# Performance work log

Measured on AMD Instinct MI355X. Metric: run time of the kernel, lower is better.

Reference implementation:

```python
import jax, jax.numpy as jnp
import numpy as np

NU, NI, ED, H = 30000, 10000, 64, 4
D = ED * H            # fusion_dim = 256
N = NU + NI           # total graph nodes
E = 100000            # edges
B = 8192              # scored (user, wine) pairs
NST, SD = 4, 64       # side tokens / side token dim
NEG = -1e30


def setup_inputs():
    key = jax.random.key(0)
    ks = iter(jax.random.split(key, 64))

    def w(*shape):
        return jax.random.normal(next(ks), shape, jnp.float32) * 0.05

    return {
        "user": jax.random.randint(next(ks), (B,), 0, NU),
        "wine": jax.random.randint(next(ks), (B,), 0, NI),
        "edge_index": jax.random.randint(next(ks), (2, E), 0, N),
        "keep_edge": jax.random.uniform(next(ks), (E,)) > 0.2,   # edge_dropout keep mask
        "node_mask": jax.random.uniform(next(ks), (N,)) < 0.2,   # mask-autoencoding mask
        "user_emb": w(NU, ED),
        "wine_emb": w(NI, ED),
        "up_w": w(ED, D), "up_b": w(D),
        "wp_w": w(ED, D), "wp_b": w(D),
        "sf_proj_w": w(SD, D), "sf_proj_b": w(D),
        "sf_q_w": w(D, D), "sf_q_b": w(D),
        "sf_k_w": w(D, D), "sf_k_b": w(D),
        "sf_v_w": w(D, D), "sf_v_b": w(D),
        "sf_o_w": w(D, D), "sf_o_b": w(D),
        "sf_fc_w": w(2 * D, D), "sf_fc_b": w(D),
        "g_w": w(D, D), "g_b": w(D),
        "t_q_w": w(D, H * D), "t_q_b": w(H * D),
        "t_k_w": w(D, H * D), "t_k_b": w(H * D),
        "t_v_w": w(D, H * D), "t_v_b": w(H * D),
        "t_skip_w": w(D, D), "t_skip_b": w(D),
        "fc_w": w(2 * D, 1), "fc_b": w(1),
        "ae_w": w(D, D), "ae_b": w(D),
        "ep_w": w(2 * D, 1), "ep_b": w(1),
        "wine_side_features": jax.random.normal(next(ks), (NI, NST, SD), jnp.float32),
    }


def _forward(user, wine, edge_index, keep_edge, node_mask,
             user_emb, wine_emb, up_w, up_b, wp_w, wp_b,
             sf_proj_w, sf_proj_b, sf_q_w, sf_q_b, sf_k_w, sf_k_b,
             sf_v_w, sf_v_b, sf_o_w, sf_o_b, sf_fc_w, sf_fc_b,
             g_w, g_b, t_q_w, t_q_b, t_k_w, t_k_b, t_v_w, t_v_b,
             t_skip_w, t_skip_b, fc_w, fc_b, ae_w, ae_b, ep_w, ep_b,
             wine_side_features):
    u_proj = user_emb @ up_w + up_b                       # [NU, D]
    w_proj = wine_emb @ wp_w + wp_b                       # [NI, D]

    # WineSideFusion: single-head attention of wine embedding over side tokens
    side = wine_side_features @ sf_proj_w + sf_proj_b     # [NI, T, D]
    q = w_proj @ sf_q_w + sf_q_b                          # [NI, D]
    k = side @ sf_k_w + sf_k_b                            # [NI, T, D]
    v = side @ sf_v_w + sf_v_b
    attn = jax.nn.softmax(jnp.einsum('nd,ntd->nt', q, k) / jnp.sqrt(jnp.float32(D)), axis=-1)
    ao = jnp.einsum('nt,ntd->nd', attn, v) @ sf_o_w + sf_o_b
    fused = jnp.concatenate([w_proj, ao], axis=1) @ sf_fc_w + sf_fc_b

    x = jnp.concatenate([u_proj, fused], axis=0)          # [N, D]
    src, dst = edge_index[0], edge_index[1]
    ew = keep_edge.astype(x.dtype)                        # edge dropout as 0/1 weights

    # GCNConv (add self loops, symmetric norm)
    deg = jax.ops.segment_sum(ew, dst, num_segments=N) + 1.0
    dinv = jax.lax.rsqrt(deg)
    norm = dinv[src] * dinv[dst] * ew                     # [E]
    xw = x @ g_w                                          # [N, D]
    agg = jax.ops.segment_sum(xw[src] * norm[:, None], dst, num_segments=N)
    x = agg + xw * (dinv * dinv)[:, None] + g_b

    # TransformerConv(heads=H, concat=False): mean over heads + skip
    qh = (x @ t_q_w + t_q_b).reshape(N, H, D)
    kh = (x @ t_k_w + t_k_b).reshape(N, H, D)
    vh = (x @ t_v_w + t_v_b).reshape(N, H, D)
    logits = jnp.einsum('ehd,ehd->eh', qh[dst], kh[src]) / jnp.sqrt(jnp.float32(D))
    logits = jnp.where(keep_edge[:, None], logits, NEG)
    m = jax.ops.segment_max(logits, dst, num_segments=N)  # [N, H]
    m = jnp.where(m < NEG / 2, 0.0, m)                    # guard empty segments
    e = jnp.exp(logits - m[dst]) * ew[:, None]            # [E, H]
    den = jax.ops.segment_sum(e, dst, num_segments=N)     # [N, H]
    num = jax.ops.segment_sum(e[:, :, None] * vh[src], dst, num_segments=N)  # [N, H, D]
    attn_out = num / jnp.maximum(den, 1e-16)[:, :, None]
    x = attn_out.mean(axis=1) + x @ t_skip_w + t_skip_b   # [N, D]

    # Masked autoencoding: masked rows are zeroed, then autoencoded -> recon = bias
    maskf = node_mask.astype(x.dtype)
    recon = ae_b                                          # 0 @ ae_w + ae_b
    diff = recon[None, :] - x                             # [N, D]
    recon_loss = jnp.sum(maskf[:, None] * diff * diff) / (jnp.sum(maskf) * D)

    u_out = x[user]                                       # [B, D]
    w_out = x[wine + NU]                                  # [B, D]
    pair = jnp.concatenate([u_out, w_out], axis=1)        # [B, 2D]

    edge_score = jax.nn.sigmoid(pair @ ep_w + ep_b)       # [B, 1]
    edge_pred_loss = jnp.mean((edge_score - 1.0) ** 2)

    score = jax.nn.sigmoid((pair @ fc_w + fc_b).squeeze(-1)) * 4.0 + 1.0  # [B]
    return score, recon_loss, edge_pred_loss


def reference(user, wine, edge_index, keep_edge, node_mask,
              user_emb, wine_emb, up_w, up_b, wp_w, wp_b,
              sf_proj_w, sf_proj_b, sf_q_w, sf_q_b, sf_k_w, sf_k_b,
              sf_v_w, sf_v_b, sf_o_w, sf_o_b, sf_fc_w, sf_fc_b,
              g_w, g_b, t_q_w, t_q_b, t_k_w, t_k_b, t_v_w, t_v_b,
              t_skip_w, t_skip_b, fc_w, fc_b, ae_w, ae_b, ep_w, ep_b,
              wine_side_features):
    return _forward(user, wine, edge_index, keep_edge, node_mask,
                    user_emb, wine_emb, up_w, up_b, wp_w, wp_b,
                    sf_proj_w, sf_proj_b, sf_q_w, sf_q_b, sf_k_w, sf_k_b,
                    sf_v_w, sf_v_b, sf_o_w, sf_o_b, sf_fc_w, sf_fc_b,
                    g_w, g_b, t_q_w, t_q_b, t_k_w, t_k_b, t_v_w, t_v_b,
                    t_skip_w, t_skip_b, fc_w, fc_b, ae_w, ae_b, ep_w, ep_b,
                    wine_side_features)
```

## Files before the change

### kernel.cpp

```cpp
#include <hip/hip_runtime.h>
#include <stdint.h>

typedef unsigned short u16;
typedef unsigned char u8;
typedef __attribute__((ext_vector_type(8))) short bf16x8;
typedef __attribute__((ext_vector_type(4))) float f32x4;

#define NU_C 30000
#define NI_C 10000
#define N_C  40000
#define E_C  100000
#define B_C  8192

static __device__ __forceinline__ float bf2f(u16 u) {
    union { unsigned int i; float f; } c; c.i = ((unsigned int)u) << 16; return c.f;
}
static __device__ __forceinline__ u16 f2bf(float f) {
    union { float f; unsigned int i; } c; c.f = f;
    return (u16)((c.i + 0x7FFFu + ((c.i >> 16) & 1u)) >> 16);
}
static __device__ __forceinline__ float wave_sum(float v) {
#pragma unroll
    for (int off = 32; off > 0; off >>= 1) v += __shfl_xor(v, off);
    return v;
}

__global__ void zero_kernel(unsigned int* p, int n) {
    int i = blockIdx.x * 256 + threadIdx.x;
    if (i < n) p[i] = 0u;
}
__global__ void fillval_kernel(float* p, int n, float v) {
    int i = blockIdx.x * 256 + threadIdx.x;
    if (i < n) p[i] = v;
}

__global__ void detect_kernel(const unsigned int* a, int n, int* flag) {
    int i = blockIdx.x * 256 + threadIdx.x;
    if (i >= n) return;
    unsigned int v = a[i];
    int f = 0;
    if (v > 1u) f |= 1;
    if (v != 0u && v != 0x3F800000u) f |= 2;
    if (f) atomicOr(flag, f);
}
__global__ void conv_mask_kernel(const void* raw, u8* outm, int n, const int* flag) {
    int i = blockIdx.x * 256 + threadIdx.x;
    if (i >= n) return;
    const int f = *flag;
    u8 r;
    if ((f & 1) == 0)      r = ((const int*)raw)[i] != 0;
    else if ((f & 2) == 0) r = ((const float*)raw)[i] != 0.f;
    else                   r = ((const u8*)raw)[i] != 0;
    outm[i] = r;
}

__global__ void conv3_kernel(const float* __restrict__ a, int na4,
                             const float* __restrict__ b, int nb4,
                             const float* __restrict__ c, int nc4,
                             u16* __restrict__ oa, u16* __restrict__ ob, u16* __restrict__ oc)
{
    int tot = na4 + nb4 + nc4;
    for (int i = blockIdx.x * 256 + threadIdx.x; i < tot; i += gridDim.x * 256) {
        const float* s; u16* o; int j = i;
        if (j < na4) { s = a; o = oa; }
        else if ((j -= na4) < nb4) { s = b; o = ob; }
        else { j -= nb4; s = c; o = oc; }
        float4 v = *(const float4*)&s[(size_t)j * 4];
        ushort4 r;
        r.x = f2bf(v.x); r.y = f2bf(v.y); r.z = f2bf(v.z); r.w = f2bf(v.w);
        *(ushort4*)&o[(size_t)j * 4] = r;
    }
}

#define WT_ELEMS 1359872
__device__ const int wd_prefix[23] = {0,16384,32768,49152,114688,180224,245760,311296,442368,
    507904,573440,638976,704512,770048,835584,901120,966656,1032192,1097728,1163264,1228800,
    1294336,1359872};
__device__ const u8  wd_src[22]  = {0,1,2,3,4,5,6,7,8,9,10,11,12,10,11,12,10,11,12,10,11,12};
__device__ const short wd_ldw[22]= {256,256,256,256,256,256,256,256,256,256,
    1024,1024,1024,1024,1024,1024,1024,1024,1024,1024,1024,1024};
__device__ const short wd_coff[22]={0,0,0,0,0,0,0,0,0,0, 0,0,0, 256,256,256, 512,512,512, 768,768,768};
__device__ const short wd_kmask[22]={63,63,63,255,255,255,255,511,255,255,
    255,255,255,255,255,255,255,255,255,255,255,255};
__device__ const u8  wd_ksh[22] = {6,6,6,8,8,8,8,9,8,8, 8,8,8,8,8,8,8,8,8,8,8,8};

__global__ __launch_bounds__(256)
void wtrans_kernel(const float* w0, const float* w1, const float* w2, const float* w3,
                   const float* w4, const float* w5, const float* w6, const float* w7,
                   const float* w8, const float* w9, const float* w10, const float* w11,
                   const float* w12, u16* __restrict__ WT)
{
    int idx = blockIdx.x * 256 + threadIdx.x;
    if (idx >= WT_ELEMS) return;
    int d = 0;
    while (wd_prefix[d + 1] <= idx) ++d;
    const int local = idx - wd_prefix[d];
    const int k = local & wd_kmask[d];
    const int n = local >> wd_ksh[d];
    const float* s;
    switch (wd_src[d]) {
        case 0: s = w0; break; case 1: s = w1; break; case 2: s = w2; break;
        case 3: s = w3; break; case 4: s = w4; break; case 5: s = w5; break;
        case 6: s = w6; break; case 7: s = w7; break; case 8: s = w8; break;
        case 9: s = w9; break; case 10: s = w10; break; case 11: s = w11; break;
        default: s = w12; break;
    }
    WT[idx] = f2bf(s[(size_t)k * wd_ldw[d] + wd_coff[d] + n]);
}

__global__ void prep_bias_kernel(const float* sfk_b, const float* sfv_b,
                                 const float* tq_b, const float* tk_b, const float* tv_b,
                                 float* kvb, float* qkvb)
{
    int i = blockIdx.x * 256 + threadIdx.x;
    if (i < 512) kvb[i] = i < 256 ? sfk_b[i] : sfv_b[i - 256];
    if (i < 3072) {
        int h = i / 768, j = i - h * 768;
        qkvb[i] = j < 256 ? tq_b[h * 256 + j]
                : (j < 512 ? tk_b[h * 256 + j - 256] : tv_b[h * 256 + j - 512]);
    }
}

template <typename OT>
__global__ __launch_bounds__(256)
void mgemm_kernel(const u16* __restrict__ A, int lda,
                  const u16* __restrict__ WT,
                  const float* __restrict__ bias,
                  OT* __restrict__ C, int ldc,
                  int M, int N, int K)
{
    __shared__ __align__(16) u16 As[128][72];
    __shared__ __align__(16) u16 Bs[128][72];
    const int t = threadIdx.x;
    const int wid = t >> 6, lane = t & 63;
    const int wr = wid >> 1, wc = wid & 1;
    const int lr = lane & 15, lg = lane >> 4;
    const int gx = gridDim.x;
    const int nwg = gx * gridDim.y;
    const int orig = blockIdx.y * gx + blockIdx.x;
    const int q8 = nwg >> 3, r8 = nwg & 7;
    const int xcd = orig & 7, oidx = orig >> 3;
    const int swz = (xcd < r8 ? xcd * (q8 + 1) : r8 * (q8 + 1) + (xcd - r8) * q8) + oidx;
    const int row0 = (swz / gx) * 128, col0 = (swz % gx) * 128;
    const int sr = t >> 1, sh = (t & 1) * 32;
    f32x4 acc[4][4] = {};

    for (int k0 = 0; k0 < K; k0 += 64) {
        const int gr = row0 + sr;
        if (gr < M) {
            const u16* ap = &A[(size_t)gr * lda + k0 + sh];
#pragma unroll
            for (int j = 0; j < 4; ++j)
                *(bf16x8*)&As[sr][sh + j * 8] = *(const bf16x8*)&ap[j * 8];
        } else {
            const bf16x8 z = {0, 0, 0, 0, 0, 0, 0, 0};
#pragma unroll
            for (int j = 0; j < 4; ++j)
                *(bf16x8*)&As[sr][sh + j * 8] = z;
        }
        {
            const u16* bp = &WT[(size_t)(col0 + sr) * K + k0 + sh];
#pragma unroll
            for (int j = 0; j < 4; ++j)
                *(bf16x8*)&Bs[sr][sh + j * 8] = *(const bf16x8*)&bp[j * 8];
        }
        __syncthreads();
#pragma unroll
        for (int kk = 0; kk < 2; ++kk) {
            bf16x8 af[4], bfr[4];
#pragma unroll
            for (int m = 0; m < 4; ++m)
                af[m] = *(const bf16x8*)&As[wr * 64 + m * 16 + lr][kk * 32 + lg * 8];
#pragma unroll
            for (int n = 0; n < 4; ++n)
                bfr[n] = *(const bf16x8*)&Bs[wc * 64 + n * 16 + lr][kk * 32 + lg * 8];
#pragma unroll
            for (int m = 0; m < 4; ++m)
#pragma unroll
                for (int n = 0; n < 4; ++n)
                    acc[m][n] = __builtin_amdgcn_mfma_f32_16x16x32_bf16(af[m], bfr[n], acc[m][n], 0, 0, 0);
        }
        __syncthreads();
    }
#pragma unroll
    for (int m = 0; m < 4; ++m) {
#pragma unroll
        for (int r = 0; r < 4; ++r) {
            int row = row0 + wr * 64 + m * 16 + lg * 4 + r;
            if (row >= M) continue;
#pragma unroll
            for (int n = 0; n < 4; ++n) {
                int col = col0 + wc * 64 + n * 16 + lr;
                float v = acc[m][n][r];
                if (bias) v += bias[col];
                if constexpr (sizeof(OT) == 4) C[(size_t)row * ldc + col] = v;
                else C[(size_t)row * ldc + col] = f2bf(v);
            }
        }
    }
}

__global__ __launch_bounds__(256)
void side_attn_kernel(const u16* __restrict__ q, const u16* __restrict__ kv,
                      u16* __restrict__ ao, int NI)
{
    const int wid = threadIdx.x >> 6, lane = threadIdx.x & 63;
    const int n = blockIdx.x * 4 + wid;
    if (n >= NI) return;
    const ushort4 qu = *(const ushort4*)&q[(size_t)n * 256 + lane * 4];
    const float q0 = bf2f(qu.x), q1 = bf2f(qu.y), q2 = bf2f(qu.z), q3 = bf2f(qu.w);
    float logit[4];
#pragma unroll
    for (int tk = 0; tk < 4; ++tk) {
        const ushort4 ku = *(const ushort4*)&kv[((size_t)n * 4 + tk) * 512 + lane * 4];
        float p = q0 * bf2f(ku.x) + q1 * bf2f(ku.y) + q2 * bf2f(ku.z) + q3 * bf2f(ku.w);
        logit[tk] = wave_sum(p) * (1.f / 16.f);
    }
    float mx = fmaxf(fmaxf(logit[0], logit[1]), fmaxf(logit[2], logit[3]));
    float e[4], den = 0.f;
#pragma unroll
    for (int tk = 0; tk < 4; ++tk) { e[tk] = __expf(logit[tk] - mx); den += e[tk]; }
    const float inv = 1.f / den;
    float o0 = 0.f, o1 = 0.f, o2 = 0.f, o3 = 0.f;
#pragma unroll
    for (int tk = 0; tk < 4; ++tk) {
        const ushort4 vu = *(const ushort4*)&kv[((size_t)n * 4 + tk) * 512 + 256 + lane * 4];
        const float w = e[tk] * inv;
        o0 = fmaf(w, bf2f(vu.x), o0); o1 = fmaf(w, bf2f(vu.y), o1);
        o2 = fmaf(w, bf2f(vu.z), o2); o3 = fmaf(w, bf2f(vu.w), o3);
    }
    ushort4 o;
    o.x = f2bf(o0); o.y = f2bf(o1); o.z = f2bf(o2); o.w = f2bf(o3);
    *(ushort4*)&ao[(size_t)n * 256 + lane * 4] = o;
}

__global__ void degw_kernel(const int* __restrict__ dst, const u8* __restrict__ keep,
                            float* __restrict__ degw, int E)
{
    int e = blockIdx.x * 256 + threadIdx.x;
    if (e >= E) return;
    if (keep[e]) atomicAdd(&degw[dst[e]], 1.f);
}

__global__ void dinv_kernel(const float* __restrict__ degw, float* __restrict__ dinv, int N)
{
    int n = blockIdx.x * 256 + threadIdx.x;
    if (n < N) dinv[n] = rsqrtf(degw[n] + 1.f);
}

__global__ void count_kernel(const int* __restrict__ dst, int* __restrict__ cnt, int E)
{
    int e = blockIdx.x * 256 + threadIdx.x;
    if (e < E) atomicAdd(&cnt[dst[e]], 1);
}

__global__ __launch_bounds__(1024)
void scan_kernel(const int* __restrict__ cnt, int* __restrict__ rs, int n)
{
    __shared__ int wsum[17];
    __shared__ int s_run;
    const int t = threadIdx.x, lane = t & 63, wid = t >> 6;
    if (t == 0) s_run = 0;
    __syncthreads();
    for (int base = 0; base < n; base += 1024) {
        int i = base + t;
        int v = (i < n) ? cnt[i] : 0;
        int x = v;
#pragma unroll
        for (int off = 1; off < 64; off <<= 1) {
            int y = __shfl_up(x, off);
            if (lane >= off) x += y;
        }
        if (lane == 63) wsum[wid] = x;
        __syncthreads();
        if (t == 0) {
            int a = 0;
            for (int j = 0; j < 16; ++j) { int tmp = wsum[j]; wsum[j] = a; a += tmp; }
            wsum[16] = a;
        }
        __syncthreads();
        if (i < n) rs[i] = s_run + wsum[wid] + x - v;
        __syncthreads();
        if (t == 0) s_run += wsum[16];
        __syncthreads();
    }
    if (t == 0) rs[n] = s_run;
}

__global__ void fill_kernel(const int* __restrict__ dst, const int* __restrict__ rs,
                            int* __restrict__ cursor, int* __restrict__ eid, int E)
{
    int e = blockIdx.x * 256 + threadIdx.x;
    if (e >= E) return;
    int d = dst[e];
    int p = atomicAdd(&cursor[d], 1);
    eid[rs[d] + p] = e;
}

__global__ void sort_kernel(const int* __restrict__ rs, int* __restrict__ eid, int N)
{
    int n = blockIdx.x * 256 + threadIdx.x;
    if (n >= N) return;
    const int b = rs[n], len = rs[n + 1] - b;
    for (int i = 1; i < len; ++i) {
        int key = eid[b + i];
        int j = i - 1;
        while (j >= 0 && eid[b + j] > key) { eid[b + j + 1] = eid[b + j]; --j; }
        eid[b + j + 1] = key;
    }
}

__global__ __launch_bounds__(256)
void gcn_kernel(const u16* __restrict__ xw, const int* __restrict__ src,
                const u8* __restrict__ keep,
                const int* __restrict__ rs, const int* __restrict__ eid,
                const float* __restrict__ dinv, const float* __restrict__ gb,
                u16* __restrict__ xout, int N)
{
    const int n = blockIdx.x;
    const int d = threadIdx.x;
    const float di = dinv[n];
    float acc = bf2f(xw[(size_t)n * 256 + d]) * di * di;
    const int e0 = rs[n], e1 = rs[n + 1];
    for (int i = e0; i < e1; ++i) {
        const int e = eid[i];
        if (!keep[e]) continue;
        const int s = src[e];
        acc = fmaf(bf2f(xw[(size_t)s * 256 + d]), dinv[s] * di, acc);
    }
    xout[(size_t)n * 256 + d] = f2bf(acc + gb[d]);
}

__global__ __launch_bounds__(256)
void tconv_head_kernel(const u16* __restrict__ qkv,
                       const int* __restrict__ src, const u8* __restrict__ keep,
                       const int* __restrict__ rs, const int* __restrict__ eid,
                       float* __restrict__ xacc, int N)
{
    const int wid = threadIdx.x >> 6, lane = threadIdx.x & 63;
    const int n = blockIdx.x * 4 + wid;
    if (n >= N) return;
    const ushort4 qu = *(const ushort4*)&qkv[(size_t)n * 768 + lane * 4];
    const float q0 = bf2f(qu.x), q1 = bf2f(qu.y), q2 = bf2f(qu.z), q3 = bf2f(qu.w);
    const int e0 = rs[n], e1 = rs[n + 1];
    float m = -1e30f, den = 0.f;
    float a0 = 0.f, a1 = 0.f, a2 = 0.f, a3 = 0.f;
    for (int i = e0; i < e1; ++i) {
        const int e = eid[i];
        if (!keep[e]) continue;
        const int s = src[e];
        const ushort4 ku = *(const ushort4*)&qkv[(size_t)s * 768 + 256 + lane * 4];
        float p = q0 * bf2f(ku.x) + q1 * bf2f(ku.y) + q2 * bf2f(ku.z) + q3 * bf2f(ku.w);
        p = wave_sum(p);
        const float lg = p * (1.f / 16.f);
        if (lg > m) {
            const float sc = __expf(m - lg);
            den *= sc; a0 *= sc; a1 *= sc; a2 *= sc; a3 *= sc;
            m = lg;
        }
        const float w = __expf(lg - m);
        den += w;
        const ushort4 vu = *(const ushort4*)&qkv[(size_t)s * 768 + 512 + lane * 4];
        a0 = fmaf(w, bf2f(vu.x), a0); a1 = fmaf(w, bf2f(vu.y), a1);
        a2 = fmaf(w, bf2f(vu.z), a2); a3 = fmaf(w, bf2f(vu.w), a3);
    }
    const float inv = 0.25f / fmaxf(den, 1e-16f);
    float4* p4 = (float4*)&xacc[(size_t)n * 256 + lane * 4];
    float4 cur = *p4;
    cur.x += a0 * inv; cur.y += a1 * inv; cur.z += a2 * inv; cur.w += a3 * inv;
    *p4 = cur;
}

__global__ __launch_bounds__(256)
void recon_kernel(const float* __restrict__ x, const u8* __restrict__ mask,
                  const float* __restrict__ aeb,
                  float* __restrict__ rblkS, float* __restrict__ rblkC, int N)
{
    const int total = N * 256;
    float s = 0.f, c = 0.f;
    for (int idx = blockIdx.x * 256 + threadIdx.x; idx < total; idx += gridDim.x * 256) {
        const int n = idx >> 8, d = idx & 255;
        if (mask[n]) {
            const float diff = aeb[d] - x[idx];
            s = fmaf(diff, diff, s);
            if (d == 0) c += 1.f;
        }
    }
    s = wave_sum(s); c = wave_sum(c);
    __shared__ float ss[4], cc[4];
    const int lane = threadIdx.x & 63, wid = threadIdx.x >> 6;
    if (lane == 0) { ss[wid] = s; cc[wid] = c; }
    __syncthreads();
    if (threadIdx.x == 0) {
        rblkS[blockIdx.x] = ss[0] + ss[1] + ss[2] + ss[3];
        rblkC[blockIdx.x] = cc[0] + cc[1] + cc[2] + cc[3];
    }
}

__global__ __launch_bounds__(256)
void score_kernel(const float* __restrict__ x, const int* __restrict__ user,
                  const int* __restrict__ wine,
                  const float* __restrict__ epw, const float* __restrict__ epb,
                  const float* __restrict__ fcw, const float* __restrict__ fcb,
                  float* __restrict__ out, float* __restrict__ sblk, int B)
{
    __shared__ float sep[4];
    const int wid = threadIdx.x >> 6, lane = threadIdx.x & 63;
    const int b = blockIdx.x * 4 + wid;
    if (b < B) {
        const size_t u = (size_t)user[b];
        const size_t w = (size_t)wine[b] + NU_C;
        const float4 xu = *(const float4*)&x[u * 256 + lane * 4];
        const float4 xw = *(const float4*)&x[w * 256 + lane * 4];
        const float4 e1 = *(const float4*)&epw[lane * 4];
        const float4 e2 = *(const float4*)&epw[256 + lane * 4];
        const float4 f1 = *(const float4*)&fcw[lane * 4];
        const float4 f2 = *(const float4*)&fcw[256 + lane * 4];
        float pep = xu.x * e1.x + xu.y * e1.y + xu.z * e1.z + xu.w * e1.w
                  + xw.x * e2.x + xw.y * e2.y + xw.z * e2.z + xw.w * e2.w;
        float pfc = xu.x * f1.x + xu.y * f1.y + xu.z * f1.z + xu.w * f1.w
                  + xw.x * f2.x + xw.y * f2.y + xw.z * f2.z + xw.w * f2.w;
        pep = wave_sum(pep); pfc = wave_sum(pfc);
        if (lane == 0) {
            const float es = 1.f / (1.f + __expf(-(pep + epb[0])));
            sep[wid] = (es - 1.f) * (es - 1.f);
            out[b] = 1.f / (1.f + __expf(-(pfc + fcb[0]))) * 4.f + 1.f;
        }
    } else if (lane == 0) {
        sep[wid] = 0.f;
    }
    __syncthreads();
    if (threadIdx.x == 0) sblk[blockIdx.x] = sep[0] + sep[1] + sep[2] + sep[3];
}

__global__ __launch_bounds__(1024)
void final_reduce_kernel(const float* __restrict__ rblkS, const float* __restrict__ rblkC,
                         const float* __restrict__ sblk, float* __restrict__ out, int B)
{
    const int t = threadIdx.x, lane = t & 63, wid = t >> 6;
    float s = rblkS[t] + rblkS[t + 1024];
    float c = rblkC[t] + rblkC[t + 1024];
    float p = sblk[t] + sblk[t + 1024];
    s = wave_sum(s); c = wave_sum(c); p = wave_sum(p);
    __shared__ float ss[16], cc[16], pp[16];
    if (lane == 0) { ss[wid] = s; cc[wid] = c; pp[wid] = p; }
    __syncthreads();
    if (t == 0) {
        float S = 0.f, C = 0.f, P = 0.f;
        for (int i = 0; i < 16; ++i) { S += ss[i]; C += cc[i]; P += pp[i]; }
        out[B] = S / (C * 256.f);
        out[B + 1] = P / (float)B;
    }
}

extern "C" void kernel_launch(void* const* d_in, const int* in_sizes, int n_in,
                              void* d_out, int out_size, void* d_ws, size_t ws_size,
                              hipStream_t stream)
{
    const int* user = (const int*)d_in[0];
    const int* wine = (const int*)d_in[1];
    const int* e_src = (const int*)d_in[2];
    const int* e_dst = e_src + E_C;
    const void* keep_raw  = d_in[3];
    const void* nmask_raw = d_in[4];
    const float* user_emb = (const float*)d_in[5];
    const float* wine_emb = (const float*)d_in[6];
    const float* up_w = (const float*)d_in[7];
    const float* up_b = (const float*)d_in[8];
    const float* wp_w = (const float*)d_in[9];
    const float* wp_b = (const float*)d_in[10];
    const float* sf_proj_w = (const float*)d_in[11];
    const float* sf_proj_b = (const float*)d_in[12];
    const float* sf_q_w = (const float*)d_in[13];
    const float* sf_q_b = (const float*)d_in[14];
    const float* sf_k_w = (const float*)d_in[15];
    const float* sf_k_b = (const float*)d_in[16];
    const float* sf_v_w = (const float*)d_in[17];
    const float* sf_v_b = (const float*)d_in[18];
    const float* sf_o_w = (const float*)d_in[19];
    const float* sf_o_b = (const float*)d_in[20];
    const float* sf_fc_w = (const float*)d_in[21];
    const float* sf_fc_b = (const float*)d_in[22];
    const float* g_w = (const float*)d_in[23];
    const float* g_b = (const float*)d_in[24];
    const float* t_q_w = (const float*)d_in[25];
    const float* t_q_b = (const float*)d_in[26];
    const float* t_k_w = (const float*)d_in[27];
    const float* t_k_b = (const float*)d_in[28];
    const float* t_v_w = (const float*)d_in[29];
    const float* t_v_b = (const float*)d_in[30];
    const float* t_skip_w = (const float*)d_in[31];
    const float* t_skip_b = (const float*)d_in[32];
    const float* fc_w = (const float*)d_in[33];
    const float* fc_b = (const float*)d_in[34];
    const float* ae_b = (const float*)d_in[36];
    const float* ep_w = (const float*)d_in[37];
    const float* ep_b = (const float*)d_in[38];
    const float* wsf = (const float*)d_in[39];
    float* out = (float*)d_out;
    char* ws = (char*)d_ws;

    size_t off = 0;
    auto take = [&](size_t b) { size_t r = off; off += (b + 255) & ~(size_t)255; return r; };
    const size_t o_xb     = take((size_t)N_C * 256 * 2);
    const size_t o_cnt    = take((size_t)N_C * 4);
    const size_t o_degw   = take((size_t)N_C * 4);
    const size_t o_cursor = take((size_t)N_C * 4);
    const size_t o_scal   = take(256);
    const size_t o_rowst  = take((size_t)(N_C + 1) * 4);
    const size_t o_dinv   = take((size_t)N_C * 4);
    const size_t o_eid    = take((size_t)E_C * 4);
    const size_t o_kmask  = take((size_t)E_C);
    const size_t o_nmask  = take((size_t)N_C);
    const size_t o_rblkS  = take(2048 * 4);
    const size_t o_rblkC  = take(2048 * 4);
    const size_t o_sblk   = take(2048 * 4);
    const size_t o_wt     = take((size_t)WT_ELEMS * 2);
    const size_t o_bias   = take(3584 * 4);
    const size_t ARENA    = 102400000;
    const size_t o_arena  = take(ARENA);
    const size_t NEED = off;

    if (ws_size < NEED) {
        fillval_kernel<<<dim3((out_size + 255) / 256), 256, 0, stream>>>(
            out, out_size, (float)((double)ws_size / (1024.0 * 1024.0)));
        return;
    }

    u16*   xb     = (u16*)  (ws + o_xb);
    int*   cnt    = (int*)  (ws + o_cnt);
    float* degw   = (float*)(ws + o_degw);
    int*   cursor = (int*)  (ws + o_cursor);
    int*   flag   = (int*)  (ws + o_scal);
    int*   rowst  = (int*)  (ws + o_rowst);
    float* dinvb  = (float*)(ws + o_dinv);
    int*   eid    = (int*)  (ws + o_eid);
    u8*    kmask  = (u8*)   (ws + o_kmask);
    u8*    nmaskb = (u8*)   (ws + o_nmask);
    float* rblkS  = (float*)(ws + o_rblkS);
    float* rblkC  = (float*)(ws + o_rblkC);
    float* sblk   = (float*)(ws + o_sblk);
    u16*   WT     = (u16*)  (ws + o_wt);
    float* kvb    = (float*)(ws + o_bias);
    float* qkvb   = kvb + 512;

    u16* wt_up   = WT + 0;
    u16* wt_wp   = WT + 16384;
    u16* wt_proj = WT + 32768;
    u16* wt_sfq  = WT + 49152;
    u16* wt_sfkv = WT + 114688;
    u16* wt_sfo  = WT + 245760;
    u16* wt_sffc = WT + 311296;
    u16* wt_g    = WT + 442368;
    u16* wt_skip = WT + 507904;
    u16* wt_qkv  = WT + 573440;

    u16* ue16  = (u16*)(ws + o_arena);
    u16* we16  = (u16*)(ws + o_arena + 3840000);
    u16* wsf16 = (u16*)(ws + o_arena + 5120000);
    u16* cat   = (u16*)(ws + o_arena + 10240000);
    u16* side  = (u16*)(ws + o_arena + 20480000);
    u16* qbuf  = (u16*)(ws + o_arena + 40960000);
    u16* kvbuf = (u16*)(ws + o_arena + 46080000);
    u16* aobuf = (u16*)(ws + o_arena + 87040000);
    u16* xw    = (u16*)(ws + o_arena);
    u16* qkvh  = (u16*)(ws + o_arena);
    float* xacc = (float*)(ws + o_arena + 61440000);

    const int zero_words = (3 * N_C * 4 + 256) / 4;
    zero_kernel<<<dim3((zero_words + 255) / 256), 256, 0, stream>>>((unsigned int*)cnt, zero_words);

    detect_kernel<<<dim3((E_C / 4 + 255) / 256), 256, 0, stream>>>((const unsigned int*)keep_raw, E_C / 4, flag);
    conv_mask_kernel<<<dim3((E_C + 255) / 256), 256, 0, stream>>>(keep_raw, kmask, E_C, flag);
    conv_mask_kernel<<<dim3((N_C + 255) / 256), 256, 0, stream>>>(nmask_raw, nmaskb, N_C, flag);

    conv3_kernel<<<dim3(2048), 256, 0, stream>>>(user_emb, NU_C * 16, wine_emb, NI_C * 16,
                                                 wsf, N_C * 16, ue16, we16, wsf16);
    wtrans_kernel<<<dim3(WT_ELEMS / 256), 256, 0, stream>>>(up_w, wp_w, sf_proj_w, sf_q_w,
        sf_k_w, sf_v_w, sf_o_w, sf_fc_w, g_w, t_skip_w, t_q_w, t_k_w, t_v_w, WT);
    prep_bias_kernel<<<dim3(12), 256, 0, stream>>>(sf_k_b, sf_v_b, t_q_b, t_k_b, t_v_b, kvb, qkvb);

    mgemm_kernel<u16><<<dim3(2, 235), 256, 0, stream>>>(ue16, 64, wt_up, up_b, xb, 256, NU_C, 256, 64);
    mgemm_kernel<u16><<<dim3(2, 79), 256, 0, stream>>>(we16, 64, wt_wp, wp_b, cat, 512, NI_C, 256, 64);
    mgemm_kernel<u16><<<dim3(2, 313), 256, 0, stream>>>(wsf16, 64, wt_proj, sf_proj_b, side, 256, N_C, 256, 64);
    mgemm_kernel<u16><<<dim3(2, 79), 256, 0, stream>>>(cat, 512, wt_sfq, sf_q_b, qbuf, 256, NI_C, 256, 256);
    mgemm_kernel<u16><<<dim3(4, 313), 256, 0, stream>>>(side, 256, wt_sfkv, kvb, kvbuf, 512, N_C, 512, 256);
    side_attn_kernel<<<dim3(2500), 256, 0, stream>>>(qbuf, kvbuf, aobuf, NI_C);
    mgemm_kernel<u16><<<dim3(2, 79), 256, 0, stream>>>(aobuf, 256, wt_sfo, sf_o_b, cat + 256, 512, NI_C, 256, 256);
    mgemm_kernel<u16><<<dim3(2, 79), 256, 0, stream>>>(cat, 512, wt_sffc, sf_fc_b, xb + (size_t)NU_C * 256, 256, NI_C, 256, 512);

    degw_kernel<<<dim3((E_C + 255) / 256), 256, 0, stream>>>(e_dst, kmask, degw, E_C);
    dinv_kernel<<<dim3((N_C + 255) / 256), 256, 0, stream>>>(degw, dinvb, N_C);
    count_kernel<<<dim3((E_C + 255) / 256), 256, 0, stream>>>(e_dst, cnt, E_C);
    scan_kernel<<<dim3(1), 1024, 0, stream>>>(cnt, rowst, N_C);
    fill_kernel<<<dim3((E_C + 255) / 256), 256, 0, stream>>>(e_dst, rowst, cursor, eid, E_C);
    sort_kernel<<<dim3((N_C + 255) / 256), 256, 0, stream>>>(rowst, eid, N_C);

    mgemm_kernel<u16><<<dim3(2, 313), 256, 0, stream>>>(xb, 256, wt_g, nullptr, xw, 256, N_C, 256, 256);
    gcn_kernel<<<dim3(N_C), 256, 0, stream>>>(xw, e_src, kmask, rowst, eid, dinvb, g_b, xb, N_C);

    mgemm_kernel<float><<<dim3(2, 313), 256, 0, stream>>>(xb, 256, wt_skip, t_skip_b, xacc, 256, N_C, 256, 256);
    for (int h = 0; h < 4; ++h) {
        mgemm_kernel<u16><<<dim3(6, 313), 256, 0, stream>>>(xb, 256, wt_qkv + h * 196608,
                                                            qkvb + h * 768, qkvh, 768, N_C, 768, 256);
        tconv_head_kernel<<<dim3(N_C / 4), 256, 0, stream>>>(qkvh, e_src, kmask, rowst, eid, xacc, N_C);
    }

    recon_kernel<<<dim3(2048), 256, 0, stream>>>(xacc, nmaskb, ae_b, rblkS, rblkC, N_C);
    score_kernel<<<dim3(2048), 256, 0, stream>>>(xacc, user, wine, ep_w, ep_b, fc_w, fc_b, out, sblk, B_C);
    final_reduce_kernel<<<dim3(1), 1024, 0, stream>>>(rblkS, rblkC, sblk, out, B_C);
}
```

Measured before the change: 735.3 us.

## Prefetch next K tile into registers and XOR-swizzle LDS layout in GEMM

The bf16 MFMA GEMM now issues the global loads for the next K tile into registers before computing on the current LDS tile, then writes them to shared memory after a barrier. This overlaps global memory latency with compute. The padded [128][72] LDS arrays are also replaced by unpadded buffers with an XOR swizzle on 16-byte groups, which avoids bank conflicts while cutting LDS use. Out-of-range rows now load from a clamped address and are replaced with zeros. The cost is more registers held across the loop and an extra barrier per iteration.

```diff
diff --git a/kernel.cpp b/kernel.cpp
--- a/kernel.cpp
+++ b/kernel.cpp
@@ -129,8 +129,8 @@
                   OT* __restrict__ C, int ldc,
                   int M, int N, int K)
 {
-    __shared__ __align__(16) u16 As[128][72];
-    __shared__ __align__(16) u16 Bs[128][72];
+    __shared__ __align__(16) u16 As[8192];
+    __shared__ __align__(16) u16 Bs[8192];
     const int t = threadIdx.x;
     const int wid = t >> 6, lane = t & 63;
     const int wr = wid >> 1, wc = wid & 1;
@@ -140,48 +140,68 @@
     const int orig = blockIdx.y * gx + blockIdx.x;
     const int q8 = nwg >> 3, r8 = nwg & 7;
     const int xcd = orig & 7, oidx = orig >> 3;
-    const int swz = (xcd < r8 ? xcd * (q8 + 1) : r8 * (q8 + 1) + (xcd - r8) * q8) + oidx;
-    const int row0 = (swz / gx) * 128, col0 = (swz % gx) * 128;
-    const int sr = t >> 1, sh = (t & 1) * 32;
+    const int swzb = (xcd < r8 ? xcd * (q8 + 1) : r8 * (q8 + 1) + (xcd - r8) * q8) + oidx;
+    const int row0 = (swzb / gx) * 128, col0 = (swzb % gx) * 128;
+
+    const int sr = t >> 1;
+    const int sg0 = (t & 1) * 4;
+    const bool avalid = (row0 + sr) < M;
+    const u16* aptr = &A[(size_t)min(row0 + sr, M - 1) * lda];
+    const u16* bptr = &WT[(size_t)(col0 + sr) * K];
+    const int swr = (sr & 7);
     f32x4 acc[4][4] = {};
-
-    for (int k0 = 0; k0 < K; k0 += 64) {
-        const int gr = row0 + sr;
-        if (gr < M) {
-            const u16* ap = &A[(size_t)gr * lda + k0 + sh];
-#pragma unroll
-            for (int j = 0; j < 4; ++j)
-                *(bf16x8*)&As[sr][sh + j * 8] = *(const bf16x8*)&ap[j * 8];
-        } else {
-            const bf16x8 z = {0, 0, 0, 0, 0, 0, 0, 0};
-#pragma unroll
-            for (int j = 0; j < 4; ++j)
-                *(bf16x8*)&As[sr][sh + j * 8] = z;
-        }
-        {
-            const u16* bp = &WT[(size_t)(col0 + sr) * K + k0 + sh];
-#pragma unroll
-            for (int j = 0; j < 4; ++j)
-                *(bf16x8*)&Bs[sr][sh + j * 8] = *(const bf16x8*)&bp[j * 8];
-        }
-        __syncthreads();
+    bf16x8 ra[4], rb[4];
+    const bf16x8 z = {0, 0, 0, 0, 0, 0, 0, 0};
+
+    auto gload = [&](int k0) {
+#pragma unroll
+        for (int j = 0; j < 4; ++j) {
+            ra[j] = avalid ? *(const bf16x8*)&aptr[k0 + (sg0 + j) * 8] : z;
+            rb[j] = *(const bf16x8*)&bptr[k0 + (sg0 + j) * 8];
+        }
+    };
+    auto swrite = [&]() {
+#pragma unroll
+        for (int j = 0; j < 4; ++j) {
+            const int g = (sg0 + j) ^ swr;
+            *(bf16x8*)&As[(sr * 8 + g) * 8] = ra[j];
+            *(bf16x8*)&Bs[(sr * 8 + g) * 8] = rb[j];
+        }
+    };
+    auto compute = [&]() {
 #pragma unroll
         for (int kk = 0; kk < 2; ++kk) {
             bf16x8 af[4], bfr[4];
 #pragma unroll
-            for (int m = 0; m < 4; ++m)
-                af[m] = *(const bf16x8*)&As[wr * 64 + m * 16 + lr][kk * 32 + lg * 8];
-#pragma unroll
-            for (int n = 0; n < 4; ++n)
-                bfr[n] = *(const bf16x8*)&Bs[wc * 64 + n * 16 + lr][kk * 32 + lg * 8];
+            for (int m = 0; m < 4; ++m) {
+                const int r = wr * 64 + m * 16 + lr;
+                af[m] = *(const bf16x8*)&As[(r * 8 + ((kk * 4 + lg) ^ (r & 7))) * 8];
+            }
+#pragma unroll
+            for (int n = 0; n < 4; ++n) {
+                const int r = wc * 64 + n * 16 + lr;
+                bfr[n] = *(const bf16x8*)&Bs[(r * 8 + ((kk * 4 + lg) ^ (r & 7))) * 8];
+            }
 #pragma unroll
             for (int m = 0; m < 4; ++m)
 #pragma unroll
                 for (int n = 0; n < 4; ++n)
                     acc[m][n] = __builtin_amdgcn_mfma_f32_16x16x32_bf16(af[m], bfr[n], acc[m][n], 0, 0, 0);
         }
+    };
+
+    gload(0);
+    swrite();
+    __syncthreads();
+    for (int k0 = 64; k0 < K; k0 += 64) {
+        gload(k0);
+        compute();
         __syncthreads();
-    }
+        swrite();
+        __syncthreads();
+    }
+    compute();
+
 #pragma unroll
     for (int m = 0; m < 4; ++m) {
 #pragma unroll
```

New measurement: 806.9 us. +9.7%, slower.
